# Kernel tuning notes

Hardware: AMD Instinct MI355X
Metric: run time of the kernel (lower is better)

## Reference

```python
import jax, jax.numpy as jnp
import numpy as np

N_NODES = 100000


def _gcn_conv(x, src, dst, W, b, n):
    # PyG GCNConv: x' = D^-1/2 (A + I) D^-1/2 (x W) + b, edges flow src -> dst
    h = x @ W                                        # [n, out]
    ones = jnp.ones(src.shape[0], dtype=h.dtype)
    deg = jax.ops.segment_sum(ones, dst, num_segments=n) + 1.0  # +1 for self-loop
    dis = jax.lax.rsqrt(deg)                         # deg >= 1, no inf handling needed
    norm = dis[src] * dis[dst]                       # [E]
    agg = jax.ops.segment_sum(norm[:, None] * h[src], dst, num_segments=n)
    agg = agg + (dis * dis)[:, None] * h             # self-loop term, norm_ii = 1/deg_i
    return agg + b


def setup_inputs() -> dict:
    key = jax.random.key(0)
    k1, k2, k3, k4, k5, k6, k7, k8 = jax.random.split(key, 8)
    in_c, hid = 128, 64
    x = jax.random.normal(k1, (N_NODES, in_c), dtype=jnp.float32)
    edge_index = jax.random.randint(k2, (2, 1600000), 0, N_NODES, dtype=jnp.int64)
    s1 = 1.0 / np.sqrt(in_c)
    s2 = 1.0 / np.sqrt(hid)
    W1 = jax.random.uniform(k3, (in_c, hid), jnp.float32, -s1, s1)
    b1 = jnp.zeros((hid,), jnp.float32)
    W2 = jax.random.uniform(k4, (hid, hid), jnp.float32, -s2, s2)
    b2 = jnp.zeros((hid,), jnp.float32)
    Wl = jax.random.uniform(k5, (hid, 1), jnp.float32, -s2, s2)
    bl = jax.random.uniform(k6, (1,), jnp.float32, -s2, s2)
    return {"x": x, "edge_index": edge_index, "W1": W1, "b1": b1,
            "W2": W2, "b2": b2, "Wl": Wl, "bl": bl}


def reference(x, edge_index, W1, b1, W2, b2, Wl, bl):
    src, dst = edge_index[0], edge_index[1]
    n = x.shape[0]
    h = jax.nn.relu(_gcn_conv(x, src, dst, W1, b1, n))
    # dropout is identity in eval mode
    h = _gcn_conv(h, src, dst, W2, b2, n)
    return jax.nn.sigmoid(h @ Wl + bl)               # [n, 1]
```

## Files before the change

kernel.cpp:

```cpp
#include <hip/hip_runtime.h>
#include <hip/hip_bf16.h>


#define EPB 4096
#define NBMAX 512

typedef __attribute__((ext_vector_type(8))) short bf16x8;
typedef __attribute__((ext_vector_type(4))) float f32x4;

__device__ __forceinline__ unsigned short f2b(float f) {
    unsigned u = __builtin_bit_cast(unsigned, f);
    u += 0x7fffu + ((u >> 16) & 1u);
    return (unsigned short)(u >> 16);
}
__device__ __forceinline__ float b2f(unsigned short h) {
    unsigned u = (unsigned)h << 16;
    return __builtin_bit_cast(float, u);
}


__global__ __launch_bounds__(256) void bcount_k(
    const int* __restrict__ dst, int* __restrict__ bucket_cnt, int E, int nbuckets) {
    __shared__ int lh[NBMAX];
    int t = threadIdx.x;
    for (int i = t; i < nbuckets; i += 256) lh[i] = 0;
    __syncthreads();
    int e0 = blockIdx.x * EPB;
    int cnt = min(EPB, E - e0);
    for (int i = t; i < cnt; i += 256) atomicAdd(&lh[dst[e0 + i] >> 8], 1);
    __syncthreads();
    for (int i = t; i < nbuckets; i += 256)
        if (lh[i]) atomicAdd(&bucket_cnt[i], lh[i]);
}

__global__ __launch_bounds__(512) void bscan_k(
    const int* __restrict__ cnt, int* __restrict__ base, int* __restrict__ cur, int nb) {
    __shared__ int s[512];
    int t = threadIdx.x;
    int v = (t < nb) ? cnt[t] : 0;
    s[t] = v; __syncthreads();
    #pragma unroll
    for (int off = 1; off < 512; off <<= 1) {
        int u = (t >= off) ? s[t - off] : 0;
        __syncthreads();
        s[t] += u;
        __syncthreads();
    }
    if (t < nb) { int e = s[t] - v; base[t] = e; cur[t] = e; }
    if (t == nb - 1) base[nb] = s[t];
}

__global__ __launch_bounds__(256) void partition_k(
    const int* __restrict__ src, const int* __restrict__ dst,
    int* __restrict__ bucket_cur, int* __restrict__ stage, int E, int nbuckets) {
    __shared__ int ls[EPB];
    __shared__ int ld[EPB];
    __shared__ int lhist[NBMAX];
    __shared__ int lbase[NBMAX];
    int e0 = blockIdx.x * EPB;
    int cnt = min(EPB, E - e0);
    int t = threadIdx.x;
    for (int i = t; i < cnt; i += 256) { ls[i] = src[e0 + i]; ld[i] = dst[e0 + i]; }
    for (int b = t; b < nbuckets; b += 256) lhist[b] = 0;
    __syncthreads();
    for (int i = t; i < cnt; i += 256) atomicAdd(&lhist[ld[i] >> 8], 1);
    __syncthreads();
    for (int b = t; b < nbuckets; b += 256) {
        int c = lhist[b];
        lbase[b] = (c > 0) ? atomicAdd(&bucket_cur[b], c) : 0;
        lhist[b] = 0;
    }
    __syncthreads();
    for (int i = t; i < cnt; i += 256) {
        int d  = ld[i];
        int b  = d >> 8;
        int off = atomicAdd(&lhist[b], 1);
        stage[lbase[b] + off] = ls[i] | ((d & 255) << 17);
    }
}

__global__ __launch_bounds__(256) void bucket_place_k(
    const int* __restrict__ stage, const int* __restrict__ bucket_base,
    int* __restrict__ row_start, float* __restrict__ dis,
    int* __restrict__ csr_src, int n, int nbuckets) {
    __shared__ int lh[256];
    __shared__ int ss[256];
    __shared__ int lcur[256];
    int b = blockIdx.x;
    int t = threadIdx.x;
    int ebeg = bucket_base[b], eend = bucket_base[b + 1];
    int node0 = b << 8;

    lh[t] = 0;
    __syncthreads();
    for (int e = ebeg + t; e < eend; e += 256)
        atomicAdd(&lh[(stage[e] >> 17) & 255], 1);
    __syncthreads();

    int cnt = lh[t];
    ss[t] = cnt;
    __syncthreads();
    #pragma unroll
    for (int off = 1; off < 256; off <<= 1) {
        int u = (t >= off) ? ss[t - off] : 0;
        __syncthreads();
        ss[t] += u;
        __syncthreads();
    }
    int excl = ss[t] - cnt;
    int node = node0 + t;
    if (node < n) {
        row_start[node] = ebeg + excl;
        dis[node] = rsqrtf((float)cnt + 1.0f);
    }
    lcur[t] = ebeg + excl;
    if (b == nbuckets - 1 && t == 0) row_start[n] = eend;
    __syncthreads();

    for (int e = ebeg + t; e < eend; e += 256) {
        int p = stage[e];
        int pos = atomicAdd(&lcur[(p >> 17) & 255], 1);
        csr_src[pos] = p & 0x1FFFF;
    }
}

__global__ void wfrag_k(const float* __restrict__ W1, const float* __restrict__ W2,
                        unsigned short* __restrict__ fw1, unsigned short* __restrict__ fw2,
                        const float* __restrict__ b2, const float* __restrict__ Wl,
                        const float* __restrict__ bl, float* __restrict__ c0,
                        int* __restrict__ bcnt) {
    int gid = blockIdx.x * blockDim.x + threadIdx.x;
    if (gid <= NBMAX) bcnt[gid] = 0;
    if (blockIdx.x == 0 && threadIdx.x < 64) {
        float v = b2[threadIdx.x] * Wl[threadIdx.x];
        #pragma unroll
        for (int m = 32; m >= 1; m >>= 1) v += __shfl_xor(v, m);
        if (threadIdx.x == 0) c0[0] = v + bl[0];
    }
    if (gid < 8192) {
        int f = gid >> 9, rem = gid & 511;
        int l = rem >> 3, i = rem & 7;
        int ks = f >> 2, ct = f & 3;
        int k = ks * 32 + ((l >> 4) << 3) + i;
        int c = ct * 16 + (l & 15);
        fw1[gid] = f2b(W1[k * 64 + c]);
    } else if (gid < 8192 + 4096) {
        int g = gid - 8192;
        int f = g >> 9, rem = g & 511;
        int l = rem >> 3, i = rem & 7;
        int ks = f >> 2, ct = f & 3;
        int k = ks * 32 + ((l >> 4) << 3) + i;
        int c = ct * 16 + (l & 15);
        fw2[g] = f2b(W2[k * 64 + c]);
    }
}

template <int K, bool BF16IN, int EPI>
__global__ __launch_bounds__(256) void mfma_gemm_k(
    const void* __restrict__ Xv, const unsigned short* __restrict__ FW,
    const float* __restrict__ dis, unsigned short* __restrict__ Y,
    const float* __restrict__ Wl, float* __restrict__ z, int n) {
    constexpr int KS = K / 32;
    int wave   = (int)((blockIdx.x * blockDim.x + threadIdx.x) >> 6);
    int lane   = threadIdx.x & 63;
    int nwaves = (int)((gridDim.x * blockDim.x) >> 6);
    int ntiles = n >> 4;

    bf16x8 bfrag[KS][4];
    #pragma unroll
    for (int ks = 0; ks < KS; ++ks)
        #pragma unroll
        for (int ct = 0; ct < 4; ++ct)
            bfrag[ks][ct] = *reinterpret_cast<const bf16x8*>(FW + ((ks * 4 + ct) << 9) + (lane << 3));

    int rb = lane & 15;
    int kb = (lane >> 4) << 3;

    float wl0, wl1, wl2, wl3;
    if (EPI == 1) {
        int fq = lane & 15;
        wl0 = Wl[fq]; wl1 = Wl[16 + fq]; wl2 = Wl[32 + fq]; wl3 = Wl[48 + fq];
    }

    for (int tile = wave; tile < ntiles; tile += nwaves) {
        int row = (tile << 4) + rb;
        f32x4 acc[4];
        #pragma unroll
        for (int ct = 0; ct < 4; ++ct) acc[ct] = (f32x4){0.f, 0.f, 0.f, 0.f};

        #pragma unroll
        for (int ks = 0; ks < KS; ++ks) {
            bf16x8 af;
            if (BF16IN) {
                af = *reinterpret_cast<const bf16x8*>(
                    (const unsigned short*)Xv + (size_t)row * K + ks * 32 + kb);
            } else {
                const float* p = (const float*)Xv + (size_t)row * K + ks * 32 + kb;
                float4 u = *reinterpret_cast<const float4*>(p);
                float4 v = *reinterpret_cast<const float4*>(p + 4);
                af[0] = (short)f2b(u.x); af[1] = (short)f2b(u.y);
                af[2] = (short)f2b(u.z); af[3] = (short)f2b(u.w);
                af[4] = (short)f2b(v.x); af[5] = (short)f2b(v.y);
                af[6] = (short)f2b(v.z); af[7] = (short)f2b(v.w);
            }
            #pragma unroll
            for (int ct = 0; ct < 4; ++ct)
                acc[ct] = __builtin_amdgcn_mfma_f32_16x16x32_bf16(af, bfrag[ks][ct], acc[ct], 0, 0, 0);
        }

        int orow0 = (tile << 4) + ((lane >> 4) << 2);
        if (EPI == 0) {
            int ocol = lane & 15;
            float dv0 = dis[orow0], dv1 = dis[orow0 + 1], dv2 = dis[orow0 + 2], dv3 = dis[orow0 + 3];
            #pragma unroll
            for (int ct = 0; ct < 4; ++ct) {
                Y[(size_t)(orow0 + 0) * 64 + ct * 16 + ocol] = f2b(acc[ct][0] * dv0);
                Y[(size_t)(orow0 + 1) * 64 + ct * 16 + ocol] = f2b(acc[ct][1] * dv1);
                Y[(size_t)(orow0 + 2) * 64 + ct * 16 + ocol] = f2b(acc[ct][2] * dv2);
                Y[(size_t)(orow0 + 3) * 64 + ct * 16 + ocol] = f2b(acc[ct][3] * dv3);
            }
        } else {
            #pragma unroll
            for (int reg = 0; reg < 4; ++reg) {
                float p = acc[0][reg] * wl0 + acc[1][reg] * wl1
                        + acc[2][reg] * wl2 + acc[3][reg] * wl3;
                p += __shfl_xor(p, 1); p += __shfl_xor(p, 2);
                p += __shfl_xor(p, 4); p += __shfl_xor(p, 8);
                if ((lane & 15) == 0) {
                    int row = orow0 + reg;
                    z[row] = p * dis[row];
                }
            }
        }
    }

    if (EPI == 0) {
        for (int r = (ntiles << 4) + wave; r < n; r += nwaves) {
            float a = 0.f;
            int c = lane;
            for (int k = 0; k < K; ++k) {
                float xv = BF16IN ? b2f(((const unsigned short*)Xv)[(size_t)r * K + k])
                                  : ((const float*)Xv)[(size_t)r * K + k];
                int f  = (k >> 5) * 4 + (c >> 4);
                int lf = (c & 15) + (((k & 31) >> 3) << 4);
                int i  = k & 7;
                a = fmaf(xv, b2f(FW[(f << 9) + (lf << 3) + i]), a);
            }
            Y[(size_t)r * 64 + c] = f2b(a * dis[r]);
        }
    }
}

__global__ __launch_bounds__(256) void gather_k(
    const int* __restrict__ row_start, const int* __restrict__ csr_src,
    const float* __restrict__ dis, const unsigned short* __restrict__ tp,
    const float* __restrict__ b, unsigned short* __restrict__ outbuf, int n) {
    int node = (int)((blockIdx.x * blockDim.x + threadIdx.x) >> 6);
    int lane = threadIdx.x & 63;
    if (node >= n) return;
    int beg = row_start[node], end = row_start[node + 1];
    float dd = dis[node];
    float a0 = b2f(tp[(size_t)node * 64 + lane]);
    float a1 = 0.f, a2 = 0.f, a3 = 0.f, a4 = 0.f, a5 = 0.f, a6 = 0.f, a7 = 0.f;

    for (int base = beg; base < end; base += 64) {
        int rem = end - base;
        int cnt = rem < 64 ? rem : 64;
        int idx = (lane < cnt) ? csr_src[base + lane] : 0;
        int j = 0;
        for (; j + 8 <= cnt; j += 8) {
            int s0 = __shfl(idx, j + 0), s1 = __shfl(idx, j + 1);
            int s2 = __shfl(idx, j + 2), s3 = __shfl(idx, j + 3);
            int s4 = __shfl(idx, j + 4), s5 = __shfl(idx, j + 5);
            int s6 = __shfl(idx, j + 6), s7 = __shfl(idx, j + 7);
            a0 += b2f(tp[(size_t)s0 * 64 + lane]);
            a1 += b2f(tp[(size_t)s1 * 64 + lane]);
            a2 += b2f(tp[(size_t)s2 * 64 + lane]);
            a3 += b2f(tp[(size_t)s3 * 64 + lane]);
            a4 += b2f(tp[(size_t)s4 * 64 + lane]);
            a5 += b2f(tp[(size_t)s5 * 64 + lane]);
            a6 += b2f(tp[(size_t)s6 * 64 + lane]);
            a7 += b2f(tp[(size_t)s7 * 64 + lane]);
        }
        if (j + 4 <= cnt) {
            int s0 = __shfl(idx, j + 0), s1 = __shfl(idx, j + 1);
            int s2 = __shfl(idx, j + 2), s3 = __shfl(idx, j + 3);
            a0 += b2f(tp[(size_t)s0 * 64 + lane]);
            a1 += b2f(tp[(size_t)s1 * 64 + lane]);
            a2 += b2f(tp[(size_t)s2 * 64 + lane]);
            a3 += b2f(tp[(size_t)s3 * 64 + lane]);
            j += 4;
        }
        for (; j < cnt; ++j) {
            int s = __shfl(idx, j);
            a4 += b2f(tp[(size_t)s * 64 + lane]);
        }
    }

    float acc = ((a0 + a1) + (a2 + a3)) + ((a4 + a5) + (a6 + a7));
    float r = fmaf(dd, acc, b[lane]);
    outbuf[(size_t)node * 64 + lane] = f2b(fmaxf(r, 0.f));
}

__global__ __launch_bounds__(256) void gatherz_k(
    const int* __restrict__ row_start, const int* __restrict__ csr_src,
    const float* __restrict__ dis, const float* __restrict__ z,
    const float* __restrict__ c0, float* __restrict__ out, int n) {
    int i = blockIdx.x * blockDim.x + threadIdx.x;
    if (i >= n) return;
    int beg = row_start[i], end = row_start[i + 1];
    float s0 = 0.f, s1 = 0.f, s2 = 0.f, s3 = 0.f;
    int e = beg;
    for (; e + 4 <= end; e += 4) {
        s0 += z[csr_src[e + 0]];
        s1 += z[csr_src[e + 1]];
        s2 += z[csr_src[e + 2]];
        s3 += z[csr_src[e + 3]];
    }
    for (; e < end; ++e) s0 += z[csr_src[e]];
    float v = fmaf(dis[i], z[i] + ((s0 + s1) + (s2 + s3)), c0[0]);
    out[i] = 1.f / (1.f + expf(-v));
}


__global__ void relu_k(float* __restrict__ p, long long m) {
    long long i = (long long)blockIdx.x * blockDim.x + threadIdx.x;
    if (i < m) p[i] = fmaxf(p[i], 0.f);
}
__global__ void deg_init_k(float* __restrict__ deg, int n) {
    int i = blockIdx.x * blockDim.x + threadIdx.x;
    if (i < n) deg[i] = 1.0f;
}
__global__ void deg_edges_k(const int* __restrict__ dst, float* __restrict__ deg, int E) {
    int e = blockIdx.x * blockDim.x + threadIdx.x;
    if (e < E) atomicAdd(&deg[dst[e]], 1.0f);
}
__global__ void dis_k(float* __restrict__ deg, int n) {
    int i = blockIdx.x * blockDim.x + threadIdx.x;
    if (i < n) deg[i] = rsqrtf(deg[i]);
}
__global__ void init_agg_k(const float* __restrict__ t, const float* __restrict__ dis,
                           const float* __restrict__ b, float* __restrict__ agg, int n) {
    int idx = blockIdx.x * blockDim.x + threadIdx.x;
    if (idx >= n * 64) return;
    int i = idx >> 6, jj = idx & 63;
    float ds = dis[i];
    agg[idx] = ds * ds * t[idx] + b[jj];
}
__global__ __launch_bounds__(256) void agg_edges_k(
    const int* __restrict__ src, const int* __restrict__ dst,
    const float* __restrict__ dis, const float* __restrict__ t,
    float* __restrict__ agg, int E) {
    int e    = (int)((blockIdx.x * blockDim.x + threadIdx.x) >> 6);
    int lane = threadIdx.x & 63;
    if (e >= E) return;
    int s = src[e], d = dst[e];
    float w = dis[s] * dis[d];
    atomicAdd(&agg[(size_t)d * 64 + lane], w * t[(size_t)s * 64 + lane]);
}
__global__ __launch_bounds__(256) void final_k(
    const float* __restrict__ agg, const float* __restrict__ Wl,
    const float* __restrict__ bl, float* __restrict__ out, int n) {
    int node = (int)((blockIdx.x * blockDim.x + threadIdx.x) >> 6);
    int lane = threadIdx.x & 63;
    if (node >= n) return;
    float v = agg[(size_t)node * 64 + lane] * Wl[lane];
    #pragma unroll
    for (int m = 32; m >= 1; m >>= 1) v += __shfl_xor(v, m);
    if (lane == 0) out[node] = 1.f / (1.f + expf(-(v + bl[0])));
}
template <int K>
__global__ __launch_bounds__(256) void gemm_rows4_k(
    const float* __restrict__ X, const float* __restrict__ W,
    float* __restrict__ Y, int n) {
    __shared__ float Ws[K * 64];
    for (int t = threadIdx.x; t < K * 64; t += blockDim.x) Ws[t] = W[t];
    __syncthreads();
    int wave   = (int)((blockIdx.x * blockDim.x + threadIdx.x) >> 6);
    int lane   = threadIdx.x & 63;
    int nwaves = (int)((gridDim.x * blockDim.x) >> 6);
    for (int r = wave; r < n; r += nwaves) {
        const float* xr = X + (size_t)r * K;
        float acc = 0.f;
        for (int k = 0; k < K; k += 4) {
            float4 a = *reinterpret_cast<const float4*>(xr + k);
            acc = fmaf(a.x, Ws[(k + 0) * 64 + lane], acc);
            acc = fmaf(a.y, Ws[(k + 1) * 64 + lane], acc);
            acc = fmaf(a.z, Ws[(k + 2) * 64 + lane], acc);
            acc = fmaf(a.w, Ws[(k + 3) * 64 + lane], acc);
        }
        Y[(size_t)r * 64 + lane] = acc;
    }
}


extern "C" void kernel_launch(void* const* d_in, const int* in_sizes, int n_in,
                              void* d_out, int out_size, void* d_ws, size_t ws_size,
                              hipStream_t stream) {
    const float* x  = (const float*)d_in[0];
    const int*   ei = (const int*)d_in[1];
    const float* W1 = (const float*)d_in[2];
    const float* b1 = (const float*)d_in[3];
    const float* W2 = (const float*)d_in[4];
    const float* b2 = (const float*)d_in[5];
    const float* Wl = (const float*)d_in[6];
    const float* bl = (const float*)d_in[7];
    float* out = (float*)d_out;

    const int n = in_sizes[0] / 128;
    const int E = in_sizes[1] / 2;
    const int* src = ei;
    const int* dst = ei + E;

    const int B = 256;
    dim3 blk(B);
    auto align512 = [](size_t v) { return (v + 511) & ~(size_t)511; };

    char* ws = (char*)d_ws;
    size_t off = 0;
    float*          dis     = (float*)(ws + off); off = align512(off + (size_t)n * 4);
    int*            row_st  = (int*)  (ws + off); off = align512(off + (size_t)(n + 1) * 4);
    int*            bcnt    = (int*)  (ws + off); off = align512(off + (size_t)(NBMAX + 1) * 4);
    int*            bbase   = (int*)  (ws + off); off = align512(off + (size_t)(NBMAX + 1) * 4);
    int*            bcur    = (int*)  (ws + off); off = align512(off + (size_t)NBMAX * 4);
    float*          c0      = (float*)(ws + off); off = align512(off + 512);
    float*          zbuf    = (float*)(ws + off); off = align512(off + (size_t)n * 4);
    int*            csr_src = (int*)  (ws + off); off = align512(off + (size_t)E * 4);
    unsigned short* bufA16  = (unsigned short*)(ws + off); off = align512(off + (size_t)n * 64 * 2);
    unsigned short* h16     = (unsigned short*)(ws + off); off = align512(off + (size_t)n * 64 * 2);
    int*            stage   = (int*)  (ws + off); off = align512(off + (size_t)E * 4);
    unsigned short* fw1     = (unsigned short*)(ws + off); off = align512(off + 8192 * 2);
    unsigned short* fw2     = (unsigned short*)(ws + off); off = align512(off + 4096 * 2);
    size_t need_csr = off;

    const int nbuckets = (n + 255) >> 8;
    const int nebl = (E + EPB - 1) / EPB;

    if (ws_size >= need_csr && (n & 15) == 0 && nbuckets <= NBMAX && n <= (1 << 17)) {
        wfrag_k<<<48, blk, 0, stream>>>(W1, W2, fw1, fw2, b2, Wl, bl, c0, bcnt);

        bcount_k<<<nebl, blk, 0, stream>>>(dst, bcnt, E, nbuckets);
        bscan_k<<<1, 512, 0, stream>>>(bcnt, bbase, bcur, nbuckets);
        partition_k<<<nebl, blk, 0, stream>>>(src, dst, bcur, stage, E, nbuckets);
        bucket_place_k<<<nbuckets, blk, 0, stream>>>(stage, bbase, row_st, dis, csr_src, n, nbuckets);

        int gemm_blocks = ((n >> 4) + 3) / 4;

        mfma_gemm_k<128, false, 0><<<gemm_blocks, blk, 0, stream>>>(
            x, fw1, dis, bufA16, Wl, zbuf, n);
        gather_k<<<((size_t)n * 64 + B - 1) / B, blk, 0, stream>>>(
            row_st, csr_src, dis, bufA16, b1, h16, n);

        mfma_gemm_k<64, true, 1><<<gemm_blocks, blk, 0, stream>>>(
            h16, fw2, dis, (unsigned short*)nullptr, Wl, zbuf, n);
        gatherz_k<<<(n + B - 1) / B, blk, 0, stream>>>(
            row_st, csr_src, dis, zbuf, c0, out, n);
    } else {
        size_t o2 = 0;
        float* dis2 = (float*)(ws + o2); o2 = align512(o2 + (size_t)n * 4);
        float* bA   = (float*)(ws + o2); o2 += (size_t)n * 64 * 4;
        float* bB   = (float*)(ws + o2);

        deg_init_k<<<(n + B - 1) / B, blk, 0, stream>>>(dis2, n);
        deg_edges_k<<<(E + B - 1) / B, blk, 0, stream>>>(dst, dis2, E);
        dis_k<<<(n + B - 1) / B, blk, 0, stream>>>(dis2, n);

        gemm_rows4_k<128><<<2048, blk, 0, stream>>>(x, W1, bA, n);
        init_agg_k<<<((size_t)n * 64 + B - 1) / B, blk, 0, stream>>>(bA, dis2, b1, bB, n);
        agg_edges_k<<<(E + 3) / 4, blk, 0, stream>>>(src, dst, dis2, bA, bB, E);
        relu_k<<<((size_t)n * 64 + B - 1) / B, blk, 0, stream>>>(bB, (long long)n * 64);

        gemm_rows4_k<64><<<2048, blk, 0, stream>>>(bB, W2, bA, n);
        init_agg_k<<<((size_t)n * 64 + B - 1) / B, blk, 0, stream>>>(bA, dis2, b2, bB, n);
        agg_edges_k<<<(E + 3) / 4, blk, 0, stream>>>(src, dst, dis2, bA, bB, E);

        final_k<<<(n + 3) / 4, blk, 0, stream>>>(bB, Wl, bl, out, n);
    }
}
```

Baseline: 137.3 us.

## Fold W2·Wl into a vector and fuse layer-2 projection into gather

Precomputes w2l = W2 @ Wl, then has the first aggregation kernel apply ReLU, dot each node's hidden row with w2l, and write a scalar z directly. This removes the second MFMA GEMM launch and the bf16 hidden buffer write and read. It relies on layer 2 and the final linear being linear before the sigmoid, and adds a wave reduction per node in the gather kernel. The tail path for rows not divisible by 16 is dropped, which is safe because the fast path requires n to be a multiple of 16.

Measured after the change: 132.6 us. 1.04x faster.

```diff
diff --git a/kernel.cpp b/kernel.cpp
--- a/kernel.cpp
+++ b/kernel.cpp
@@ -125,7 +125,7 @@
 }
 
 __global__ void wfrag_k(const float* __restrict__ W1, const float* __restrict__ W2,
-                        unsigned short* __restrict__ fw1, unsigned short* __restrict__ fw2,
+                        unsigned short* __restrict__ fw1, float* __restrict__ w2l,
                         const float* __restrict__ b2, const float* __restrict__ Wl,
                         const float* __restrict__ bl, float* __restrict__ c0,
                         int* __restrict__ bcnt) {
@@ -137,6 +137,13 @@
         for (int m = 32; m >= 1; m >>= 1) v += __shfl_xor(v, m);
         if (threadIdx.x == 0) c0[0] = v + bl[0];
     }
+    if (blockIdx.x == 1 && threadIdx.x < 64) {
+        int k = threadIdx.x;
+        float s = 0.f;
+        #pragma unroll 8
+        for (int j = 0; j < 64; ++j) s = fmaf(W2[k * 64 + j], Wl[j], s);
+        w2l[k] = s;
+    }
     if (gid < 8192) {
         int f = gid >> 9, rem = gid & 511;
         int l = rem >> 3, i = rem & 7;
@@ -144,22 +151,13 @@
         int k = ks * 32 + ((l >> 4) << 3) + i;
         int c = ct * 16 + (l & 15);
         fw1[gid] = f2b(W1[k * 64 + c]);
-    } else if (gid < 8192 + 4096) {
-        int g = gid - 8192;
-        int f = g >> 9, rem = g & 511;
-        int l = rem >> 3, i = rem & 7;
-        int ks = f >> 2, ct = f & 3;
-        int k = ks * 32 + ((l >> 4) << 3) + i;
-        int c = ct * 16 + (l & 15);
-        fw2[g] = f2b(W2[k * 64 + c]);
-    }
-}
-
-template <int K, bool BF16IN, int EPI>
+    }
+}
+
+template <int K>
 __global__ __launch_bounds__(256) void mfma_gemm_k(
-    const void* __restrict__ Xv, const unsigned short* __restrict__ FW,
-    const float* __restrict__ dis, unsigned short* __restrict__ Y,
-    const float* __restrict__ Wl, float* __restrict__ z, int n) {
+    const float* __restrict__ X, const unsigned short* __restrict__ FW,
+    const float* __restrict__ dis, unsigned short* __restrict__ Y, int n) {
     constexpr int KS = K / 32;
     int wave   = (int)((blockIdx.x * blockDim.x + threadIdx.x) >> 6);
     int lane   = threadIdx.x & 63;
@@ -176,12 +174,6 @@
     int rb = lane & 15;
     int kb = (lane >> 4) << 3;
 
-    float wl0, wl1, wl2, wl3;
-    if (EPI == 1) {
-        int fq = lane & 15;
-        wl0 = Wl[fq]; wl1 = Wl[16 + fq]; wl2 = Wl[32 + fq]; wl3 = Wl[48 + fq];
-    }
-
     for (int tile = wave; tile < ntiles; tile += nwaves) {
         int row = (tile << 4) + rb;
         f32x4 acc[4];
@@ -190,63 +182,28 @@
 
         #pragma unroll
         for (int ks = 0; ks < KS; ++ks) {
+            const float* p = X + (size_t)row * K + ks * 32 + kb;
+            float4 u = *reinterpret_cast<const float4*>(p);
+            float4 v = *reinterpret_cast<const float4*>(p + 4);
             bf16x8 af;
-            if (BF16IN) {
-                af = *reinterpret_cast<const bf16x8*>(
-                    (const unsigned short*)Xv + (size_t)row * K + ks * 32 + kb);
-            } else {
-                const float* p = (const float*)Xv + (size_t)row * K + ks * 32 + kb;
-                float4 u = *reinterpret_cast<const float4*>(p);
-                float4 v = *reinterpret_cast<const float4*>(p + 4);
-                af[0] = (short)f2b(u.x); af[1] = (short)f2b(u.y);
-                af[2] = (short)f2b(u.z); af[3] = (short)f2b(u.w);
-                af[4] = (short)f2b(v.x); af[5] = (short)f2b(v.y);
-                af[6] = (short)f2b(v.z); af[7] = (short)f2b(v.w);
-            }
+            af[0] = (short)f2b(u.x); af[1] = (short)f2b(u.y);
+            af[2] = (short)f2b(u.z); af[3] = (short)f2b(u.w);
+            af[4] = (short)f2b(v.x); af[5] = (short)f2b(v.y);
+            af[6] = (short)f2b(v.z); af[7] = (short)f2b(v.w);
             #pragma unroll
             for (int ct = 0; ct < 4; ++ct)
                 acc[ct] = __builtin_amdgcn_mfma_f32_16x16x32_bf16(af, bfrag[ks][ct], acc[ct], 0, 0, 0);
         }
 
         int orow0 = (tile << 4) + ((lane >> 4) << 2);
-        if (EPI == 0) {
-            int ocol = lane & 15;
-            float dv0 = dis[orow0], dv1 = dis[orow0 + 1], dv2 = dis[orow0 + 2], dv3 = dis[orow0 + 3];
-            #pragma unroll
-            for (int ct = 0; ct < 4; ++ct) {
-                Y[(size_t)(orow0 + 0) * 64 + ct * 16 + ocol] = f2b(acc[ct][0] * dv0);
-                Y[(size_t)(orow0 + 1) * 64 + ct * 16 + ocol] = f2b(acc[ct][1] * dv1);
-                Y[(size_t)(orow0 + 2) * 64 + ct * 16 + ocol] = f2b(acc[ct][2] * dv2);
-                Y[(size_t)(orow0 + 3) * 64 + ct * 16 + ocol] = f2b(acc[ct][3] * dv3);
-            }
-        } else {
-            #pragma unroll
-            for (int reg = 0; reg < 4; ++reg) {
-                float p = acc[0][reg] * wl0 + acc[1][reg] * wl1
-                        + acc[2][reg] * wl2 + acc[3][reg] * wl3;
-                p += __shfl_xor(p, 1); p += __shfl_xor(p, 2);
-                p += __shfl_xor(p, 4); p += __shfl_xor(p, 8);
-                if ((lane & 15) == 0) {
-                    int row = orow0 + reg;
-                    z[row] = p * dis[row];
-                }
-            }
-        }
-    }
-
-    if (EPI == 0) {
-        for (int r = (ntiles << 4) + wave; r < n; r += nwaves) {
-            float a = 0.f;
-            int c = lane;
-            for (int k = 0; k < K; ++k) {
-                float xv = BF16IN ? b2f(((const unsigned short*)Xv)[(size_t)r * K + k])
-                                  : ((const float*)Xv)[(size_t)r * K + k];
-                int f  = (k >> 5) * 4 + (c >> 4);
-                int lf = (c & 15) + (((k & 31) >> 3) << 4);
-                int i  = k & 7;
-                a = fmaf(xv, b2f(FW[(f << 9) + (lf << 3) + i]), a);
-            }
-            Y[(size_t)r * 64 + c] = f2b(a * dis[r]);
+        int ocol  = lane & 15;
+        float dv0 = dis[orow0], dv1 = dis[orow0 + 1], dv2 = dis[orow0 + 2], dv3 = dis[orow0 + 3];
+        #pragma unroll
+        for (int ct = 0; ct < 4; ++ct) {
+            Y[(size_t)(orow0 + 0) * 64 + ct * 16 + ocol] = f2b(acc[ct][0] * dv0);
+            Y[(size_t)(orow0 + 1) * 64 + ct * 16 + ocol] = f2b(acc[ct][1] * dv1);
+            Y[(size_t)(orow0 + 2) * 64 + ct * 16 + ocol] = f2b(acc[ct][2] * dv2);
+            Y[(size_t)(orow0 + 3) * 64 + ct * 16 + ocol] = f2b(acc[ct][3] * dv3);
         }
     }
 }
@@ -254,7 +211,8 @@
 __global__ __launch_bounds__(256) void gather_k(
     const int* __restrict__ row_start, const int* __restrict__ csr_src,
     const float* __restrict__ dis, const unsigned short* __restrict__ tp,
-    const float* __restrict__ b, unsigned short* __restrict__ outbuf, int n) {
+    const float* __restrict__ b, const float* __restrict__ w2l,
+    float* __restrict__ z, int n) {
     int node = (int)((blockIdx.x * blockDim.x + threadIdx.x) >> 6);
     int lane = threadIdx.x & 63;
     if (node >= n) return;
@@ -298,8 +256,11 @@
     }
 
     float acc = ((a0 + a1) + (a2 + a3)) + ((a4 + a5) + (a6 + a7));
-    float r = fmaf(dd, acc, b[lane]);
-    outbuf[(size_t)node * 64 + lane] = f2b(fmaxf(r, 0.f));
+    float h = fmaxf(fmaf(dd, acc, b[lane]), 0.f);
+    float v = h * w2l[lane];
+    #pragma unroll
+    for (int m = 32; m >= 1; m >>= 1) v += __shfl_xor(v, m);
+    if (lane == 0) z[node] = dd * v;
 }
 
 __global__ __launch_bounds__(256) void gatherz_k(
@@ -424,20 +385,19 @@
     int*            bbase   = (int*)  (ws + off); off = align512(off + (size_t)(NBMAX + 1) * 4);
     int*            bcur    = (int*)  (ws + off); off = align512(off + (size_t)NBMAX * 4);
     float*          c0      = (float*)(ws + off); off = align512(off + 512);
+    float*          w2l     = (float*)(ws + off); off = align512(off + 64 * 4);
     float*          zbuf    = (float*)(ws + off); off = align512(off + (size_t)n * 4);
     int*            csr_src = (int*)  (ws + off); off = align512(off + (size_t)E * 4);
     unsigned short* bufA16  = (unsigned short*)(ws + off); off = align512(off + (size_t)n * 64 * 2);
-    unsigned short* h16     = (unsigned short*)(ws + off); off = align512(off + (size_t)n * 64 * 2);
     int*            stage   = (int*)  (ws + off); off = align512(off + (size_t)E * 4);
     unsigned short* fw1     = (unsigned short*)(ws + off); off = align512(off + 8192 * 2);
-    unsigned short* fw2     = (unsigned short*)(ws + off); off = align512(off + 4096 * 2);
     size_t need_csr = off;
 
     const int nbuckets = (n + 255) >> 8;
     const int nebl = (E + EPB - 1) / EPB;
 
     if (ws_size >= need_csr && (n & 15) == 0 && nbuckets <= NBMAX && n <= (1 << 17)) {
-        wfrag_k<<<48, blk, 0, stream>>>(W1, W2, fw1, fw2, b2, Wl, bl, c0, bcnt);
+        wfrag_k<<<48, blk, 0, stream>>>(W1, W2, fw1, w2l, b2, Wl, bl, c0, bcnt);
 
         bcount_k<<<nebl, blk, 0, stream>>>(dst, bcnt, E, nbuckets);
         bscan_k<<<1, 512, 0, stream>>>(bcnt, bbase, bcur, nbuckets);
@@ -446,13 +406,11 @@
 
         int gemm_blocks = ((n >> 4) + 3) / 4;
 
-        mfma_gemm_k<128, false, 0><<<gemm_blocks, blk, 0, stream>>>(
-            x, fw1, dis, bufA16, Wl, zbuf, n);
+        mfma_gemm_k<128><<<gemm_blocks, blk, 0, stream>>>(x, fw1, dis, bufA16, n);
+
         gather_k<<<((size_t)n * 64 + B - 1) / B, blk, 0, stream>>>(
-            row_st, csr_src, dis, bufA16, b1, h16, n);
-
-        mfma_gemm_k<64, true, 1><<<gemm_blocks, blk, 0, stream>>>(
-            h16, fw2, dis, (unsigned short*)nullptr, Wl, zbuf, n);
+            row_st, csr_src, dis, bufA16, b1, w2l, zbuf, n);
+
         gatherz_k<<<(n + B - 1) / B, blk, 0, stream>>>(
             row_st, csr_src, dis, zbuf, c0, out, n);
     } else {
```
